# Kernel optimization log

Measured on AMD Instinct MI355X. Metric: run time of the kernel, lower is better.

The kernel has to match this reference:

```python
import jax, jax.numpy as jnp
import numpy as np

N_NODES = 100000
N_EDGES = 800000
NUM_FEATURES = 81
NUM_BOND = 22
OUT_CHANNEL = 64
D_COORD = 3  # 'distance' rule applies to feature indices [0:3]


def setup_inputs() -> dict:
    key = jax.random.key(0)
    k1, k2, k3, k4, k5, k6 = jax.random.split(key, 6)
    features = jax.random.normal(k1, (N_NODES, NUM_FEATURES), dtype=jnp.float32)
    bond = jax.random.normal(k2, (N_EDGES, NUM_BOND), dtype=jnp.float32)
    w_s = jax.random.normal(k3, (NUM_FEATURES, OUT_CHANNEL), dtype=jnp.float32) * 0.1
    w_n = jax.random.normal(k4, (NUM_FEATURES + NUM_BOND, OUT_CHANNEL), dtype=jnp.float32) * 0.1
    src = jax.random.randint(k5, (N_EDGES,), 0, N_NODES)
    dst = jax.random.randint(k6, (N_EDGES,), 0, N_NODES)
    return {"features": features, "bond": bond, "w_s": w_s, "w_n": w_n,
            "src": src, "dst": dst}


def reference(features, bond, w_s, w_n, src, dst):
    # Gather endpoint features per edge: [E, F]
    self_f = features[src]
    nbr_f = features[dst]

    # Rule 1: 'distance' on [0:3] -> keep neighbour coords, compute L2 distance
    diff = self_f[:, :D_COORD] - nbr_f[:, :D_COORD]
    dist = jnp.sqrt(jnp.sum(diff * diff, axis=-1))      # [E]
    d = jnp.where(dist > 0, dist, jnp.float32(0.01))

    # Rule 2 (last, single-index): 'sum' on [3:]
    seg1 = nbr_f[:, :D_COORD]                           # [E, 3]
    seg2 = self_f[:, D_COORD:] + nbr_f[:, D_COORD:]     # [E, 78]

    # Distance normalization applies to the whole combined vector (pre-bond)
    combined = jnp.concatenate([seg1, seg2], axis=-1) / (d * d)[:, None]
    edge_vec = jnp.concatenate([combined, bond], axis=-1)  # [E, F + B]

    contrib = edge_vec @ w_n                            # [E, out]
    agg = jax.ops.segment_sum(contrib, src, num_segments=features.shape[0])
    return features @ w_s + agg                         # [N, out]
```

## Files before the change

### kernel.cpp

```cpp
#include <hip/hip_runtime.h>

#define N_NODES 100000
#define N_EDGES 800000
#define NF 81
#define NB 22
#define OC 64
#define SCAN_CHUNK 1024
#define SCAN_BLOCKS ((N_NODES + SCAN_CHUNK - 1) / SCAN_CHUNK)

typedef __attribute__((ext_vector_type(8))) short bf16x8;
typedef __attribute__((ext_vector_type(4))) float f32x4;

#if defined(__has_builtin)
#if __has_builtin(__builtin_amdgcn_fdot2_f32_bf16)
#define HAVE_FDOT2 1
#endif
#endif

#ifdef HAVE_FDOT2
typedef __attribute__((ext_vector_type(2))) __bf16 bfv2;
#endif

__device__ inline float dot2b(unsigned a, unsigned b, float c) {
#ifdef HAVE_FDOT2
    return __builtin_amdgcn_fdot2_f32_bf16(__builtin_bit_cast(bfv2, a),
                                           __builtin_bit_cast(bfv2, b), c, false);
#else
    return c + __uint_as_float(a << 16)         * __uint_as_float(b << 16)
             + __uint_as_float(a & 0xffff0000u) * __uint_as_float(b & 0xffff0000u);
#endif
}

__device__ inline unsigned short bfsplit(float v, float& rest) {
    const unsigned b = __float_as_uint(v);
    const unsigned short h = (unsigned short)((b + 0x7fffu + ((b >> 16) & 1u)) >> 16);
    rest = v - __uint_as_float(((unsigned)h) << 16);
    return h;
}

__global__ void k_wprep(const float* __restrict__ w_s, const float* __restrict__ w_n,
                        short* __restrict__ bt)
{
    const int tid = blockIdx.x * blockDim.x + threadIdx.x;
    if (tid >= 128 * 96) return;
    const int c = tid / 96;
    const int k = tid - c * 96;
    float v = 0.f;
    if (k < NF) v = (c < OC) ? w_s[k * OC + c] : w_n[k * OC + (c - OC)];
    float rest, dummy;
    const unsigned short h = bfsplit(v, rest);
    const unsigned short l = bfsplit(rest, dummy);
    bt[c * 96 + k]               = (short)h;
    bt[128 * 96 + c * 96 + k]    = (short)l;
}

__global__ __launch_bounds__(256) void k_node_mfma(
    const float* __restrict__ feat, const short* __restrict__ bt,
    float* __restrict__ out, float* __restrict__ pb, float4* __restrict__ xyz)
{
    __shared__ short shA[2 * 64 * 104];
    const int t    = threadIdx.x;
    const int lane = t & 63;
    const int w    = t >> 6;
    const int n0   = blockIdx.x * 64;

    const int krow = (lane >> 4) * 8;
    bf16x8 Bh[3][2], Bl[3][2];
#pragma unroll
    for (int kt = 0; kt < 3; ++kt)
#pragma unroll
        for (int c = 0; c < 2; ++c) {
            const int col = w * 32 + c * 16 + (lane & 15);
            const int off = col * 96 + kt * 32 + krow;
            Bh[kt][c] = *(const bf16x8*)(bt + off);
            Bl[kt][c] = *(const bf16x8*)(bt + 128 * 96 + off);
        }

    const long gbase = (long)n0 * NF;
    const long gmax  = (long)N_NODES * NF;
    for (int j = t; j < (64 * NF) / 4; j += 256) {
        const int flat = j * 4;
        float v[4];
        if (gbase + flat + 3 < gmax) {
            const float4 q = *(const float4*)(feat + gbase + flat);
            v[0] = q.x; v[1] = q.y; v[2] = q.z; v[3] = q.w;
        } else {
#pragma unroll
            for (int i = 0; i < 4; ++i)
                v[i] = (gbase + flat + i < gmax) ? feat[gbase + flat + i] : 0.f;
        }
#pragma unroll
        for (int i = 0; i < 4; ++i) {
            const int fi  = flat + i;
            const int row = (int)((unsigned)fi / 81u);
            const int k   = fi - row * 81;
            float rest, dummy;
            const unsigned short h = bfsplit(v[i], rest);
            const unsigned short l = bfsplit(rest, dummy);
            shA[row * 104 + k]        = (short)h;
            shA[6656 + row * 104 + k] = (short)l;
        }
    }
    for (int j = t; j < 64 * 16; j += 256) {
        const int row = j >> 4, k = NF + (j & 15);
        shA[row * 104 + k] = 0;
        shA[6656 + row * 104 + k] = 0;
    }

    if (t < 64 && n0 + t < N_NODES) {
        const float* fp = feat + (long)(n0 + t) * NF;
        xyz[n0 + t] = make_float4(fp[0], fp[1], fp[2], 0.f);
    }
    __syncthreads();

    f32x4 acc[4][2];
#pragma unroll
    for (int rt = 0; rt < 4; ++rt)
#pragma unroll
        for (int c = 0; c < 2; ++c)
            acc[rt][c] = (f32x4){0.f, 0.f, 0.f, 0.f};

#pragma unroll
    for (int kt = 0; kt < 3; ++kt) {
        bf16x8 Ah[4], Al[4];
#pragma unroll
        for (int rt = 0; rt < 4; ++rt) {
            const int o = (rt * 16 + (lane & 15)) * 104 + kt * 32 + krow;
            Ah[rt] = *(const bf16x8*)(shA + o);
            Al[rt] = *(const bf16x8*)(shA + 6656 + o);
        }
#pragma unroll
        for (int rt = 0; rt < 4; ++rt)
#pragma unroll
            for (int c = 0; c < 2; ++c) {
                f32x4 a = acc[rt][c];
                a = __builtin_amdgcn_mfma_f32_16x16x32_bf16(Ah[rt], Bh[kt][c], a, 0, 0, 0);
                a = __builtin_amdgcn_mfma_f32_16x16x32_bf16(Ah[rt], Bl[kt][c], a, 0, 0, 0);
                a = __builtin_amdgcn_mfma_f32_16x16x32_bf16(Al[rt], Bh[kt][c], a, 0, 0, 0);
                acc[rt][c] = a;
            }
    }

    const int c0    = w * 32 + (lane & 15);
    float* db       = (w < 2) ? out : pb;
    const int cbase = (w < 2) ? c0 : c0 - OC;
    const int r0    = (lane >> 4) * 4;
#pragma unroll
    for (int rt = 0; rt < 4; ++rt)
#pragma unroll
        for (int c = 0; c < 2; ++c)
#pragma unroll
            for (int reg = 0; reg < 4; ++reg) {
                const int node = n0 + rt * 16 + r0 + reg;
                if (node < N_NODES)
                    db[(long)node * OC + cbase + c * 16] = acc[rt][c][reg];
            }
}

__global__ void k_hist(const int* __restrict__ src, int* __restrict__ cnt) {
    const int e = blockIdx.x * blockDim.x + threadIdx.x;
    if (e < N_EDGES) atomicAdd(&cnt[src[e]], 1);
}

__global__ __launch_bounds__(256) void k_scan_blk(
    const int* __restrict__ cnt, int* __restrict__ row, int* __restrict__ bsum)
{
    __shared__ int sh[256];
    const int t = threadIdx.x;
    const int base = blockIdx.x * SCAN_CHUNK + t * 4;
    int c0 = 0, c1 = 0, c2 = 0, c3 = 0;
    if (base + 3 < N_NODES) {
        const int4 c = *(const int4*)(cnt + base);
        c0 = c.x; c1 = c.y; c2 = c.z; c3 = c.w;
    } else {
        if (base + 0 < N_NODES) c0 = cnt[base + 0];
        if (base + 1 < N_NODES) c1 = cnt[base + 1];
        if (base + 2 < N_NODES) c2 = cnt[base + 2];
    }
    const int s = c0 + c1 + c2 + c3;
    sh[t] = s;
    __syncthreads();
    for (int off = 1; off < 256; off <<= 1) {
        int v = sh[t];
        int a = (t >= off) ? sh[t - off] : 0;
        __syncthreads();
        sh[t] = v + a;
        __syncthreads();
    }
    const int excl = sh[t] - s;
    if (t == 255) bsum[blockIdx.x] = sh[255];
    if (base + 3 < N_NODES) {
        int4 r;
        r.x = excl; r.y = excl + c0; r.z = excl + c0 + c1; r.w = excl + c0 + c1 + c2;
        *(int4*)(row + base) = r;
    } else {
        int e = excl;
        if (base + 0 < N_NODES) { row[base + 0] = e; e += c0; }
        if (base + 1 < N_NODES) { row[base + 1] = e; e += c1; }
        if (base + 2 < N_NODES) { row[base + 2] = e; }
    }
}

__global__ void k_scan_top(int* __restrict__ bsum, int* __restrict__ row) {
    __shared__ int sh[128];
    const int t = threadIdx.x;
    const int v = (t < SCAN_BLOCKS) ? bsum[t] : 0;
    sh[t] = v;
    __syncthreads();
    for (int off = 1; off < 128; off <<= 1) {
        int x = sh[t];
        int a = (t >= off) ? sh[t - off] : 0;
        __syncthreads();
        sh[t] = x + a;
        __syncthreads();
    }
    if (t < SCAN_BLOCKS) bsum[t] = sh[t] - v;
    if (t == 127) row[N_NODES] = sh[127];
}

__global__ __launch_bounds__(256) void k_scan_add(
    int* __restrict__ row, int* __restrict__ cursor, const int* __restrict__ bsum)
{
    const int off = bsum[blockIdx.x];
    const int base = blockIdx.x * SCAN_CHUNK + threadIdx.x * 4;
    if (base + 3 < N_NODES) {
        int4 r = *(const int4*)(row + base);
        r.x += off; r.y += off; r.z += off; r.w += off;
        *(int4*)(row + base) = r;
        *(int4*)(cursor + base) = r;
    } else {
#pragma unroll
        for (int k = 0; k < 4; ++k)
            if (base + k < N_NODES) {
                const int v = row[base + k] + off;
                row[base + k] = v;
                cursor[base + k] = v;
            }
    }
}

__device__ inline unsigned pk_bf16(float a, float b) {
    const unsigned ua = (__float_as_uint(a) + 0x8000u) >> 16;
    const unsigned ub = (__float_as_uint(b) + 0x8000u) & 0xffff0000u;
    return ua | ub;
}

__global__ void k_prep(const int* __restrict__ src, const int* __restrict__ dst,
                       const float* __restrict__ bond, const float4* __restrict__ xyz,
                       int* __restrict__ cursor, unsigned* __restrict__ rec)
{
    const int e = blockIdx.x * blockDim.x + threadIdx.x;
    if (e >= N_EDGES) return;
    const int s = src[e];
    const int d = dst[e];
    const float4 a = xyz[s], b = xyz[d];
    const float dx = a.x - b.x, dy = a.y - b.y, dz = a.z - b.z;
    const float d2 = dx * dx + dy * dy + dz * dz;
    const float inv = (d2 > 0.f) ? __builtin_amdgcn_rcpf(d2) : 1.0e4f;

    float bv[NB];
    const float2* bp = (const float2*)(bond + (long)e * NB);
#pragma unroll
    for (int j = 0; j < NB / 2; ++j) {
        const float2 v = bp[j];
        bv[2 * j] = v.x; bv[2 * j + 1] = v.y;
    }

    unsigned p[11];
#pragma unroll
    for (int j = 0; j < 11; ++j) p[j] = pk_bf16(bv[2 * j], bv[2 * j + 1]);

    const int pos = atomicAdd(&cursor[s], 1);
    unsigned* r = rec + (size_t)pos * 16;
    *(uint4*)(r)     = make_uint4(p[0], p[1], p[2], p[3]);
    *(uint4*)(r + 4) = make_uint4(p[4], p[5], p[6], p[7]);
    *(uint4*)(r + 8) = make_uint4(p[8], p[9], p[10], __float_as_uint(inv));
    *(uint2*)(r + 12) = make_uint2((unsigned)d, 0u);
}

__global__ __launch_bounds__(256) void k_gather(
    const int* __restrict__ row, const unsigned* __restrict__ rec,
    const float* __restrict__ w_n, const float* __restrict__ pb,
    const float4* __restrict__ xyz, float* __restrict__ out)
{
    const int lane = threadIdx.x & 63;
    const int wid  = (int)((blockIdx.x * blockDim.x + threadIdx.x) >> 6);
    if (wid >= N_NODES) return;
    const int n = __builtin_amdgcn_readfirstlane(wid);

    unsigned wp[11];
#pragma unroll
    for (int j = 0; j < 11; ++j)
        wp[j] = pk_bf16(w_n[(NF + 2 * j) * OC + lane],
                        w_n[(NF + 2 * j + 1) * OC + lane]);
    const float w0 = w_n[0 * OC + lane];
    const float w1 = w_n[1 * OC + lane];
    const float w2 = w_n[2 * OC + lane];

    const int rs = row[n], re = row[n + 1];
    const float4 xs = xyz[n];
    const float pa = pb[(long)n * OC + lane]
                   - (xs.x * w0 + xs.y * w1 + xs.z * w2);

    float acc = 0.f;
    int i = rs;

    for (; i + 4 <= re; i += 4) {
        unsigned P[4][13];
#pragma unroll
        for (int u = 0; u < 4; ++u) {
            const unsigned* r = rec + (size_t)(i + u) * 16;
#pragma unroll
            for (int j = 0; j < 13; ++j) P[u][j] = r[j];
        }
        float pbt[4];
#pragma unroll
        for (int u = 0; u < 4; ++u)
            pbt[u] = pb[(long)(int)P[u][12] * OC + lane];
        float c[4];
#pragma unroll
        for (int u = 0; u < 4; ++u)
            c[u] = __uint_as_float(P[u][11]) * (pa + pbt[u]);
#pragma unroll
        for (int j = 0; j < 11; ++j)
#pragma unroll
            for (int u = 0; u < 4; ++u)
                c[u] = dot2b(P[u][j], wp[j], c[u]);
        acc += (c[0] + c[1]) + (c[2] + c[3]);
    }

    for (; i < re; ++i) {
        const unsigned* r = rec + (size_t)i * 16;
        unsigned p[13];
#pragma unroll
        for (int j = 0; j < 13; ++j) p[j] = r[j];
        const float pbt = pb[(long)(int)p[12] * OC + lane];
        float c = __uint_as_float(p[11]) * (pa + pbt);
#pragma unroll
        for (int j = 0; j < 11; ++j)
            c = dot2b(p[j], wp[j], c);
        acc += c;
    }

    out[(long)n * OC + lane] += acc;
}

extern "C" void kernel_launch(void* const* d_in, const int* in_sizes, int n_in,
                              void* d_out, int out_size, void* d_ws, size_t ws_size,
                              hipStream_t stream) {
    const float* feat = (const float*)d_in[0];
    const float* bond = (const float*)d_in[1];
    const float* w_s  = (const float*)d_in[2];
    const float* w_n  = (const float*)d_in[3];
    const int*   src  = (const int*)d_in[4];
    const int*   dstv = (const int*)d_in[5];
    float* out = (float*)d_out;

    char* base = (char*)d_ws;
    float*    pb     = (float*)   (base);
    float4*   xyz    = (float4*)  (base + 25600000);
    int*      row    = (int*)     (base + 27200000);
    int*      cnt    = (int*)     (base + 27600016);
    int*      cursor = (int*)     (base + 28000016);
    int*      bsum   = (int*)     (base + 28400016);
    unsigned* rec    = (unsigned*)(base + 28400576);
    short*    btw    = (short*)rec;

    hipMemsetAsync(cnt, 0, N_NODES * sizeof(int), stream);

    k_wprep   <<<48, 256, 0, stream>>>(w_s, w_n, btw);
    k_node_mfma<<<(N_NODES + 63) / 64, 256, 0, stream>>>(feat, btw, out, pb, xyz);
    k_hist    <<<(N_EDGES + 255) / 256, 256, 0, stream>>>(src, cnt);
    k_scan_blk<<<SCAN_BLOCKS, 256, 0, stream>>>(cnt, row, bsum);
    k_scan_top<<<1, 128, 0, stream>>>(bsum, row);
    k_scan_add<<<SCAN_BLOCKS, 256, 0, stream>>>(row, cursor, bsum);
    k_prep    <<<(N_EDGES + 255) / 256, 256, 0, stream>>>(src, dstv, bond, xyz,
                                                          cursor, rec);
    k_gather  <<<(N_NODES * 64 + 255) / 256, 256, 0, stream>>>(row, rec, w_n, pb,
                                                               xyz, out);
}
```

Baseline: 326.2 us.

## Record per-edge rank in histogram and split edge records into two arrays

```diff
diff --git a/kernel.cpp b/kernel.cpp
--- a/kernel.cpp
+++ b/kernel.cpp
@@ -157,9 +157,10 @@
             }
 }
 
-__global__ void k_hist(const int* __restrict__ src, int* __restrict__ cnt) {
+__global__ void k_hist(const int* __restrict__ src, int* __restrict__ cnt,
+                       int* __restrict__ rank) {
     const int e = blockIdx.x * blockDim.x + threadIdx.x;
-    if (e < N_EDGES) atomicAdd(&cnt[src[e]], 1);
+    if (e < N_EDGES) rank[e] = atomicAdd(&cnt[src[e]], 1);
 }
 
 __global__ __launch_bounds__(256) void k_scan_blk(
@@ -219,7 +220,7 @@
 }
 
 __global__ __launch_bounds__(256) void k_scan_add(
-    int* __restrict__ row, int* __restrict__ cursor, const int* __restrict__ bsum)
+    int* __restrict__ row, const int* __restrict__ bsum)
 {
     const int off = bsum[blockIdx.x];
     const int base = blockIdx.x * SCAN_CHUNK + threadIdx.x * 4;
@@ -227,15 +228,11 @@
         int4 r = *(const int4*)(row + base);
         r.x += off; r.y += off; r.z += off; r.w += off;
         *(int4*)(row + base) = r;
-        *(int4*)(cursor + base) = r;
     } else {
 #pragma unroll
         for (int k = 0; k < 4; ++k)
-            if (base + k < N_NODES) {
-                const int v = row[base + k] + off;
-                row[base + k] = v;
-                cursor[base + k] = v;
-            }
+            if (base + k < N_NODES)
+                row[base + k] += off;
     }
 }
 
@@ -245,43 +242,69 @@
     return ua | ub;
 }
 
-__global__ void k_prep(const int* __restrict__ src, const int* __restrict__ dst,
-                       const float* __restrict__ bond, const float4* __restrict__ xyz,
-                       int* __restrict__ cursor, unsigned* __restrict__ rec)
-{
-    const int e = blockIdx.x * blockDim.x + threadIdx.x;
-    if (e >= N_EDGES) return;
-    const int s = src[e];
-    const int d = dst[e];
-    const float4 a = xyz[s], b = xyz[d];
-    const float dx = a.x - b.x, dy = a.y - b.y, dz = a.z - b.z;
-    const float d2 = dx * dx + dy * dy + dz * dz;
-    const float inv = (d2 > 0.f) ? __builtin_amdgcn_rcpf(d2) : 1.0e4f;
-
-    float bv[NB];
-    const float2* bp = (const float2*)(bond + (long)e * NB);
-#pragma unroll
-    for (int j = 0; j < NB / 2; ++j) {
-        const float2 v = bp[j];
-        bv[2 * j] = v.x; bv[2 * j + 1] = v.y;
-    }
-
-    unsigned p[11];
-#pragma unroll
-    for (int j = 0; j < 11; ++j) p[j] = pk_bf16(bv[2 * j], bv[2 * j + 1]);
-
-    const int pos = atomicAdd(&cursor[s], 1);
-    unsigned* r = rec + (size_t)pos * 16;
-    *(uint4*)(r)     = make_uint4(p[0], p[1], p[2], p[3]);
-    *(uint4*)(r + 4) = make_uint4(p[4], p[5], p[6], p[7]);
-    *(uint4*)(r + 8) = make_uint4(p[8], p[9], p[10], __float_as_uint(inv));
-    *(uint2*)(r + 12) = make_uint2((unsigned)d, 0u);
+__global__ __launch_bounds__(256) void k_prep(
+    const int* __restrict__ src, const int* __restrict__ dst,
+    const float* __restrict__ bond, const float4* __restrict__ xyz,
+    const int* __restrict__ row, const int* __restrict__ rank,
+    unsigned* __restrict__ recA, unsigned* __restrict__ recB)
+{
+    const int base = blockIdx.x * 1024 + threadIdx.x;
+    bool ok[4];
+    int e[4], s[4], d[4], pos[4];
+#pragma unroll
+    for (int u = 0; u < 4; ++u) {
+        e[u]  = base + u * 256;
+        ok[u] = e[u] < N_EDGES;
+    }
+#pragma unroll
+    for (int u = 0; u < 4; ++u)
+        if (ok[u]) { s[u] = src[e[u]]; d[u] = dst[e[u]]; }
+    int rk[4];
+#pragma unroll
+    for (int u = 0; u < 4; ++u)
+        if (ok[u]) rk[u] = rank[e[u]];
+    float4 xa[4], xb[4];
+#pragma unroll
+    for (int u = 0; u < 4; ++u)
+        if (ok[u]) { xa[u] = xyz[s[u]]; xb[u] = xyz[d[u]]; }
+#pragma unroll
+    for (int u = 0; u < 4; ++u)
+        if (ok[u]) pos[u] = row[s[u]] + rk[u];
+    float inv[4];
+#pragma unroll
+    for (int u = 0; u < 4; ++u) {
+        const float dx = xa[u].x - xb[u].x, dy = xa[u].y - xb[u].y,
+                    dz = xa[u].z - xb[u].z;
+        const float d2 = dx * dx + dy * dy + dz * dz;
+        inv[u] = (d2 > 0.f) ? __builtin_amdgcn_rcpf(d2) : 1.0e4f;
+    }
+    float2 bv[4][11];
+#pragma unroll
+    for (int u = 0; u < 4; ++u)
+        if (ok[u]) {
+            const float2* bp = (const float2*)(bond + (long)e[u] * NB);
+#pragma unroll
+            for (int j = 0; j < 11; ++j) bv[u][j] = bp[j];
+        }
+#pragma unroll
+    for (int u = 0; u < 4; ++u) {
+        if (!ok[u]) continue;
+        unsigned p[11];
+#pragma unroll
+        for (int j = 0; j < 11; ++j) p[j] = pk_bf16(bv[u][j].x, bv[u][j].y);
+        unsigned* a = recA + (size_t)pos[u] * 12;
+        *(uint4*)(a)     = make_uint4(p[0], p[1], p[2], p[3]);
+        *(uint4*)(a + 4) = make_uint4(p[4], p[5], p[6], p[7]);
+        *(uint4*)(a + 8) = make_uint4(p[8], p[9], p[10], __float_as_uint(inv[u]));
+        recB[pos[u]] = (unsigned)d[u];
+    }
 }
 
 __global__ __launch_bounds__(256) void k_gather(
-    const int* __restrict__ row, const unsigned* __restrict__ rec,
-    const float* __restrict__ w_n, const float* __restrict__ pb,
-    const float4* __restrict__ xyz, float* __restrict__ out)
+    const int* __restrict__ row, const unsigned* __restrict__ recA,
+    const unsigned* __restrict__ recB, const float* __restrict__ w_n,
+    const float* __restrict__ pb, const float4* __restrict__ xyz,
+    float* __restrict__ out)
 {
     const int lane = threadIdx.x & 63;
     const int wid  = (int)((blockIdx.x * blockDim.x + threadIdx.x) >> 6);
@@ -306,17 +329,19 @@
     int i = rs;
 
     for (; i + 4 <= re; i += 4) {
-        unsigned P[4][13];
+        unsigned P[4][12];
+        unsigned db[4];
 #pragma unroll
         for (int u = 0; u < 4; ++u) {
-            const unsigned* r = rec + (size_t)(i + u) * 16;
-#pragma unroll
-            for (int j = 0; j < 13; ++j) P[u][j] = r[j];
+            const unsigned* r = recA + (size_t)(i + u) * 12;
+#pragma unroll
+            for (int j = 0; j < 12; ++j) P[u][j] = r[j];
+            db[u] = recB[i + u];
         }
         float pbt[4];
 #pragma unroll
         for (int u = 0; u < 4; ++u)
-            pbt[u] = pb[(long)(int)P[u][12] * OC + lane];
+            pbt[u] = pb[(long)(int)db[u] * OC + lane];
         float c[4];
 #pragma unroll
         for (int u = 0; u < 4; ++u)
@@ -330,11 +355,12 @@
     }
 
     for (; i < re; ++i) {
-        const unsigned* r = rec + (size_t)i * 16;
-        unsigned p[13];
-#pragma unroll
-        for (int j = 0; j < 13; ++j) p[j] = r[j];
-        const float pbt = pb[(long)(int)p[12] * OC + lane];
+        const unsigned* r = recA + (size_t)i * 12;
+        unsigned p[12];
+#pragma unroll
+        for (int j = 0; j < 12; ++j) p[j] = r[j];
+        const unsigned dbt = recB[i];
+        const float pbt = pb[(long)(int)dbt * OC + lane];
         float c = __uint_as_float(p[11]) * (pa + pbt);
 #pragma unroll
         for (int j = 0; j < 11; ++j)
@@ -361,21 +387,22 @@
     float4*   xyz    = (float4*)  (base + 25600000);
     int*      row    = (int*)     (base + 27200000);
     int*      cnt    = (int*)     (base + 27600016);
-    int*      cursor = (int*)     (base + 28000016);
-    int*      bsum   = (int*)     (base + 28400016);
-    unsigned* rec    = (unsigned*)(base + 28400576);
-    short*    btw    = (short*)rec;
+    int*      rank   = (int*)     (base + 28000016);
+    int*      bsum   = (int*)     (base + 31200016);
+    unsigned* recA   = (unsigned*)(base + 31200640);
+    unsigned* recB   = (unsigned*)(base + 69600640);
+    short*    btw    = (short*)recA;
 
     hipMemsetAsync(cnt, 0, N_NODES * sizeof(int), stream);
 
     k_wprep   <<<48, 256, 0, stream>>>(w_s, w_n, btw);
     k_node_mfma<<<(N_NODES + 63) / 64, 256, 0, stream>>>(feat, btw, out, pb, xyz);
-    k_hist    <<<(N_EDGES + 255) / 256, 256, 0, stream>>>(src, cnt);
+    k_hist    <<<(N_EDGES + 255) / 256, 256, 0, stream>>>(src, cnt, rank);
     k_scan_blk<<<SCAN_BLOCKS, 256, 0, stream>>>(cnt, row, bsum);
     k_scan_top<<<1, 128, 0, stream>>>(bsum, row);
-    k_scan_add<<<SCAN_BLOCKS, 256, 0, stream>>>(row, cursor, bsum);
-    k_prep    <<<(N_EDGES + 255) / 256, 256, 0, stream>>>(src, dstv, bond, xyz,
-                                                          cursor, rec);
-    k_gather  <<<(N_NODES * 64 + 255) / 256, 256, 0, stream>>>(row, rec, w_n, pb,
-                                                               xyz, out);
-}
+    k_scan_add<<<SCAN_BLOCKS, 256, 0, stream>>>(row, bsum);
+    k_prep    <<<(N_EDGES + 1023) / 1024, 256, 0, stream>>>(src, dstv, bond, xyz,
+                                                            row, rank, recA, recB);
+    k_gather  <<<(N_NODES * 64 + 255) / 256, 256, 0, stream>>>(row, recA, recB,
+                                                               w_n, pb, xyz, out);
+}
```

New measurement: 316.0 us. 1.03x faster.

## Write edge records in edge order and gather through a CSR permutation

Applied to the files above, without the earlier changes.

```diff
diff --git a/kernel.cpp b/kernel.cpp
--- a/kernel.cpp
+++ b/kernel.cpp
@@ -157,9 +157,10 @@
             }
 }
 
-__global__ void k_hist(const int* __restrict__ src, int* __restrict__ cnt) {
+__global__ void k_hist(const int* __restrict__ src, int* __restrict__ cnt,
+                       int* __restrict__ rank) {
     const int e = blockIdx.x * blockDim.x + threadIdx.x;
-    if (e < N_EDGES) atomicAdd(&cnt[src[e]], 1);
+    if (e < N_EDGES) rank[e] = atomicAdd(&cnt[src[e]], 1);
 }
 
 __global__ __launch_bounds__(256) void k_scan_blk(
@@ -219,7 +220,7 @@
 }
 
 __global__ __launch_bounds__(256) void k_scan_add(
-    int* __restrict__ row, int* __restrict__ cursor, const int* __restrict__ bsum)
+    int* __restrict__ row, const int* __restrict__ bsum)
 {
     const int off = bsum[blockIdx.x];
     const int base = blockIdx.x * SCAN_CHUNK + threadIdx.x * 4;
@@ -227,16 +228,18 @@
         int4 r = *(const int4*)(row + base);
         r.x += off; r.y += off; r.z += off; r.w += off;
         *(int4*)(row + base) = r;
-        *(int4*)(cursor + base) = r;
     } else {
 #pragma unroll
         for (int k = 0; k < 4; ++k)
-            if (base + k < N_NODES) {
-                const int v = row[base + k] + off;
-                row[base + k] = v;
-                cursor[base + k] = v;
-            }
-    }
+            if (base + k < N_NODES)
+                row[base + k] += off;
+    }
+}
+
+__global__ void k_perm(const int* __restrict__ src, const int* __restrict__ rank,
+                       const int* __restrict__ row, int* __restrict__ perm) {
+    const int e = blockIdx.x * blockDim.x + threadIdx.x;
+    if (e < N_EDGES) perm[row[src[e]] + rank[e]] = e;
 }
 
 __device__ inline unsigned pk_bf16(float a, float b) {
@@ -245,9 +248,10 @@
     return ua | ub;
 }
 
-__global__ void k_prep(const int* __restrict__ src, const int* __restrict__ dst,
-                       const float* __restrict__ bond, const float4* __restrict__ xyz,
-                       int* __restrict__ cursor, unsigned* __restrict__ rec)
+__global__ __launch_bounds__(256) void k_prep(
+    const int* __restrict__ src, const int* __restrict__ dst,
+    const float* __restrict__ bond, const float4* __restrict__ xyz,
+    unsigned* __restrict__ recA, unsigned* __restrict__ recB)
 {
     const int e = blockIdx.x * blockDim.x + threadIdx.x;
     if (e >= N_EDGES) return;
@@ -258,28 +262,25 @@
     const float d2 = dx * dx + dy * dy + dz * dz;
     const float inv = (d2 > 0.f) ? __builtin_amdgcn_rcpf(d2) : 1.0e4f;
 
-    float bv[NB];
+    float2 bv[11];
     const float2* bp = (const float2*)(bond + (long)e * NB);
 #pragma unroll
-    for (int j = 0; j < NB / 2; ++j) {
-        const float2 v = bp[j];
-        bv[2 * j] = v.x; bv[2 * j + 1] = v.y;
-    }
+    for (int j = 0; j < 11; ++j) bv[j] = bp[j];
 
     unsigned p[11];
 #pragma unroll
-    for (int j = 0; j < 11; ++j) p[j] = pk_bf16(bv[2 * j], bv[2 * j + 1]);
-
-    const int pos = atomicAdd(&cursor[s], 1);
-    unsigned* r = rec + (size_t)pos * 16;
+    for (int j = 0; j < 11; ++j) p[j] = pk_bf16(bv[j].x, bv[j].y);
+
+    unsigned* r = recA + (size_t)e * 12;
     *(uint4*)(r)     = make_uint4(p[0], p[1], p[2], p[3]);
     *(uint4*)(r + 4) = make_uint4(p[4], p[5], p[6], p[7]);
     *(uint4*)(r + 8) = make_uint4(p[8], p[9], p[10], __float_as_uint(inv));
-    *(uint2*)(r + 12) = make_uint2((unsigned)d, 0u);
+    recB[e] = (unsigned)d;
 }
 
 __global__ __launch_bounds__(256) void k_gather(
-    const int* __restrict__ row, const unsigned* __restrict__ rec,
+    const int* __restrict__ row, const int* __restrict__ perm,
+    const unsigned* __restrict__ recA, const unsigned* __restrict__ recB,
     const float* __restrict__ w_n, const float* __restrict__ pb,
     const float4* __restrict__ xyz, float* __restrict__ out)
 {
@@ -306,17 +307,23 @@
     int i = rs;
 
     for (; i + 4 <= re; i += 4) {
-        unsigned P[4][13];
+        int pe[4];
+#pragma unroll
+        for (int u = 0; u < 4; ++u)
+            pe[u] = __builtin_amdgcn_readfirstlane(perm[i + u]);
+        unsigned P[4][12];
+        unsigned db[4];
 #pragma unroll
         for (int u = 0; u < 4; ++u) {
-            const unsigned* r = rec + (size_t)(i + u) * 16;
-#pragma unroll
-            for (int j = 0; j < 13; ++j) P[u][j] = r[j];
+            const unsigned* r = recA + (size_t)pe[u] * 12;
+#pragma unroll
+            for (int j = 0; j < 12; ++j) P[u][j] = r[j];
+            db[u] = recB[pe[u]];
         }
         float pbt[4];
 #pragma unroll
         for (int u = 0; u < 4; ++u)
-            pbt[u] = pb[(long)(int)P[u][12] * OC + lane];
+            pbt[u] = pb[(long)(int)db[u] * OC + lane];
         float c[4];
 #pragma unroll
         for (int u = 0; u < 4; ++u)
@@ -330,11 +337,13 @@
     }
 
     for (; i < re; ++i) {
-        const unsigned* r = rec + (size_t)i * 16;
-        unsigned p[13];
-#pragma unroll
-        for (int j = 0; j < 13; ++j) p[j] = r[j];
-        const float pbt = pb[(long)(int)p[12] * OC + lane];
+        const int pe = __builtin_amdgcn_readfirstlane(perm[i]);
+        const unsigned* r = recA + (size_t)pe * 12;
+        unsigned p[12];
+#pragma unroll
+        for (int j = 0; j < 12; ++j) p[j] = r[j];
+        const unsigned dbt = recB[pe];
+        const float pbt = pb[(long)(int)dbt * OC + lane];
         float c = __uint_as_float(p[11]) * (pa + pbt);
 #pragma unroll
         for (int j = 0; j < 11; ++j)
@@ -361,21 +370,25 @@
     float4*   xyz    = (float4*)  (base + 25600000);
     int*      row    = (int*)     (base + 27200000);
     int*      cnt    = (int*)     (base + 27600016);
-    int*      cursor = (int*)     (base + 28000016);
-    int*      bsum   = (int*)     (base + 28400016);
-    unsigned* rec    = (unsigned*)(base + 28400576);
-    short*    btw    = (short*)rec;
+    int*      rank   = (int*)     (base + 28000016);
+    int*      bsum   = (int*)     (base + 31200016);
+    unsigned* recA   = (unsigned*)(base + 31200640);
+    unsigned* recB   = (unsigned*)(base + 69600640);
+    int*      perm   = (int*)     (base + 72800640);
+    short*    btw    = (short*)recA;
 
     hipMemsetAsync(cnt, 0, N_NODES * sizeof(int), stream);
 
     k_wprep   <<<48, 256, 0, stream>>>(w_s, w_n, btw);
     k_node_mfma<<<(N_NODES + 63) / 64, 256, 0, stream>>>(feat, btw, out, pb, xyz);
-    k_hist    <<<(N_EDGES + 255) / 256, 256, 0, stream>>>(src, cnt);
+    k_prep    <<<(N_EDGES + 255) / 256, 0 ? 0 : 256, 0, stream>>>(src, dstv, bond,
+                                                                  xyz, recA, recB);
+    k_hist    <<<(N_EDGES + 255) / 256, 256, 0, stream>>>(src, cnt, rank);
     k_scan_blk<<<SCAN_BLOCKS, 256, 0, stream>>>(cnt, row, bsum);
     k_scan_top<<<1, 128, 0, stream>>>(bsum, row);
-    k_scan_add<<<SCAN_BLOCKS, 256, 0, stream>>>(row, cursor, bsum);
-    k_prep    <<<(N_EDGES + 255) / 256, 256, 0, stream>>>(src, dstv, bond, xyz,
-                                                          cursor, rec);
-    k_gather  <<<(N_NODES * 64 + 255) / 256, 256, 0, stream>>>(row, rec, w_n, pb,
+    k_scan_add<<<SCAN_BLOCKS, 256, 0, stream>>>(row, bsum);
+    k_perm    <<<(N_EDGES + 255) / 256, 256, 0, stream>>>(src, rank, row, perm);
+    k_gather  <<<(N_NODES * 64 + 255) / 256, 256, 0, stream>>>(row, perm, recA,
+                                                               recB, w_n, pb,
                                                                xyz, out);
 }
```

After: 330.7 us. About the same (+1.4%).
